# Performance work log

Measured on AMD Instinct MI355X. Metric: run time of the kernel, lower is better.

The kernel has to match this reference:

```python
import jax, jax.numpy as jnp
import numpy as np

HIDDEN = 2048
N_HEADS = 16
HEAD_DIM = HIDDEN // N_HEADS
ROPE_BASE = 10000.0


def rotate_half(x):
    half = x.shape[-1] // 2
    return jnp.concatenate((-x[..., half:], x[..., :half]), axis=-1)


def rope_cos_sin(seq_len, dtype):
    inv_freq = 1.0 / (ROPE_BASE ** (jnp.arange(0, HEAD_DIM, 2, dtype=jnp.float32) / HEAD_DIM))
    pos = jnp.arange(seq_len, dtype=jnp.float32)
    freqs = jnp.einsum('i,j->ij', pos, inv_freq)  # [S, hd/2]
    emb = jnp.concatenate((freqs, freqs), axis=-1)  # [S, hd]
    return jnp.cos(emb).astype(dtype), jnp.sin(emb).astype(dtype)


def setup_inputs() -> dict:
    key = jax.random.key(0)
    ks = jax.random.split(key, 9)
    B, S, H = 2, 2048, HIDDEN
    std = 1.0 / np.sqrt(H)
    return {
        'hidden_states': jax.random.normal(ks[0], (B, S, H), dtype=jnp.float32),
        'Wq': jax.random.uniform(ks[1], (H, H), jnp.float32, -std, std),
        'bq': jax.random.uniform(ks[2], (H,), jnp.float32, -std, std),
        'Wk': jax.random.uniform(ks[3], (H, H), jnp.float32, -std, std),
        'bk': jax.random.uniform(ks[4], (H,), jnp.float32, -std, std),
        'Wv': jax.random.uniform(ks[5], (H, H), jnp.float32, -std, std),
        'bv': jax.random.uniform(ks[6], (H,), jnp.float32, -std, std),
        'Wo': jax.random.uniform(ks[7], (H, H), jnp.float32, -std, std),
        'bo': jax.random.uniform(ks[8], (H,), jnp.float32, -std, std),
    }


def reference(hidden_states, Wq, bq, Wk, bk, Wv, bv, Wo, bo):
    B, S, H = hidden_states.shape
    scale = HEAD_DIM ** -0.5

    def proj(W, b):
        # torch Linear: x @ W.T + b
        y = jnp.einsum('bsh,oh->bso', hidden_states, W) + b
        return y.reshape(B, S, N_HEADS, HEAD_DIM).transpose(0, 2, 1, 3)  # [B,nh,S,hd]

    q = proj(Wq, bq)
    k = proj(Wk, bk)
    v = proj(Wv, bv)

    cos, sin = rope_cos_sin(S, hidden_states.dtype)  # [S, hd]
    cos = cos[None, None, :, :]
    sin = sin[None, None, :, :]
    q = q * cos + rotate_half(q) * sin
    k = k * cos + rotate_half(k) * sin

    scores = jnp.einsum('bhqd,bhkd->bhqk', q, k) * scale  # [B,nh,S,S]
    probs = jax.nn.softmax(scores, axis=-1)
    ctx = jnp.einsum('bhqk,bhkd->bhqd', probs, v)
    ctx = ctx.transpose(0, 2, 1, 3).reshape(B, S, H)
    return jnp.einsum('bsh,oh->bso', ctx, Wo) + bo
```

## Files before the change

kernel.cpp:

```cpp
#include <hip/hip_runtime.h>
#include <hip/hip_bf16.h>
#include <math.h>

#define HIDDEN 2048
#define NH 16
#define HD 128
#define NB 2
#define SEQ 2048
#define K_DIM 2048

typedef unsigned int u32;
typedef unsigned short ushort_t;
typedef __bf16 bf16x8 __attribute__((ext_vector_type(8)));
typedef float f32x4 __attribute__((ext_vector_type(4)));
typedef ushort_t u16x8 __attribute__((ext_vector_type(8)));

__device__ __forceinline__ void split1(float x, unsigned short& h, unsigned short& l) {
    u32 u = __float_as_uint(x);
    u32 hr = (u + 0x7FFFu + ((u >> 16) & 1u)) >> 16;
    h = (unsigned short)hr;
    float r = x - __uint_as_float(hr << 16);
    u32 u2 = __float_as_uint(r);
    l = (unsigned short)((u2 + 0x7FFFu + ((u2 >> 16) & 1u)) >> 16);
}

__device__ __forceinline__ ushort_t bf16r(float x) {
    u32 u = __float_as_uint(x);
    return (ushort_t)((u + 0x7FFFu + ((u >> 16) & 1u)) >> 16);
}

__device__ __forceinline__ float bf2f(ushort_t u) {
    return __uint_as_float(((u32)u) << 16);
}

__device__ __forceinline__ void gl_lds16(const void* g, void* l) {
    __builtin_amdgcn_global_load_lds(
        (const __attribute__((address_space(1))) u32*)g,
        (__attribute__((address_space(3))) u32*)l, 16, 0, 0);
}

#define XG 2097152
#define WG 1048576
#define TBLK 512
__global__ void k_cvt_all(const float4* __restrict__ X, const float4* __restrict__ W0,
                          const float4* __restrict__ W1, const float4* __restrict__ W2,
                          const float4* __restrict__ Wo,
                          ushort4* __restrict__ Xh, ushort4* __restrict__ H0,
                          ushort4* __restrict__ H1, ushort4* __restrict__ H2,
                          ushort4* __restrict__ WoH, ushort4* __restrict__ WoL,
                          float* __restrict__ ct, float* __restrict__ st) {
    const int blk = blockIdx.x;
    if (blk < TBLK) {
        int idx = blk * 256 + threadIdx.x;
        int s = idx >> 6, d = idx & 63;
        double inv = pow(10000.0, -(double)d * (1.0 / 64.0));
        double ang = (double)s * inv;
        ct[idx] = (float)cos(ang);
        st[idx] = (float)sin(ang);
        return;
    }
    int idx = (blk - TBLK) * 256 + threadIdx.x;
    if (idx < XG + 3 * WG) {
        const float4* src;
        ushort4* dst;
        int off;
        if (idx < XG) { src = X; dst = Xh; off = idx; }
        else {
            int t = idx - XG;
            int m = t >> 20;
            off = t & (WG - 1);
            src = (m == 0) ? W0 : (m == 1) ? W1 : W2;
            dst = (m == 0) ? H0 : (m == 1) ? H1 : H2;
        }
        float4 x = src[off];
        ushort4 h;
        h.x = bf16r(x.x); h.y = bf16r(x.y); h.z = bf16r(x.z); h.w = bf16r(x.w);
        dst[off] = h;
    } else {
        int off = idx - XG - 3 * WG;
        float4 x = Wo[off];
        ushort4 h, l;
        split1(x.x, h.x, l.x);
        split1(x.y, h.y, l.y);
        split1(x.z, h.z, l.z);
        split1(x.w, h.w, l.w);
        WoH[off] = h;
        WoL[off] = l;
    }
}

#define BAR  __builtin_amdgcn_s_barrier()
#define VM6  asm volatile("s_waitcnt vmcnt(6)" ::: "memory")
#define VM4  asm volatile("s_waitcnt vmcnt(4)" ::: "memory")
#define VM0  asm volatile("s_waitcnt vmcnt(0)" ::: "memory")
#define PRIO1 __builtin_amdgcn_s_setprio(1)
#define PRIO0 __builtin_amdgcn_s_setprio(0)

#define QSTAGE(slot, kt) do { \
    const ushort_t* gA_ = Xh + sgA + (size_t)(kt) * 32; \
    gl_lds16(gA_, &As[slot][(w * 32) * 32]); \
    gl_lds16(gA_ + 16 * 2048, &As[slot][(w * 32 + 16) * 32]); \
    const ushort_t* gB_ = Wsel + sgB + (size_t)(kt) * 32; \
    gl_lds16(gB_, &Bs[slot][(w * 32) * 32]); \
    gl_lds16(gB_ + 16 * 2048, &Bs[slot][(w * 32 + 16) * 32]); \
} while (0)

#define QRD(AD, BD, slot) do { \
    _Pragma("unroll") for (int mf = 0; mf < 8; mf++) \
        AD[mf] = *(const bf16x8*)&As[slot][arow + mf * 512 + ccq]; \
    _Pragma("unroll") for (int nf = 0; nf < 4; nf++) \
        BD[nf] = *(const bf16x8*)&Bs[slot][brow + nf * 512 + ccq]; \
} while (0)

#define QMFMA(AD, BD) do { PRIO1; \
    _Pragma("unroll") for (int mf = 0; mf < 8; mf++) \
    _Pragma("unroll") for (int nf = 0; nf < 4; nf++) \
        acc[mf][nf] = __builtin_amdgcn_mfma_f32_16x16x32_bf16( \
            AD[mf], BD[nf], acc[mf][nf], 0, 0, 0); \
    PRIO0; } while (0)

__global__ __launch_bounds__(512, 2)
void k_gemm_qkv8(const ushort_t* __restrict__ Xh,
                 const ushort_t* __restrict__ W0, const ushort_t* __restrict__ W1,
                 const ushort_t* __restrict__ W2,
                 const float* __restrict__ b0, const float* __restrict__ b1,
                 const float* __restrict__ b2,
                 ushort_t* __restrict__ o0, ushort_t* __restrict__ o1,
                 ushort_t* __restrict__ o2) {
    __shared__ ushort_t As[4][256 * 32];
    __shared__ ushort_t Bs[4][256 * 32];
    const int tid = threadIdx.x;
    const int lane = tid & 63;
    const int w = tid >> 6;
    const int wm = w >> 2;
    const int wn = w & 3;
    const int quad = lane >> 4;
    const int l15 = lane & 15;

    const int by = blockIdx.x & 7;
    const int t = blockIdx.x >> 3;
    const int mat = t % 3;
    const int m0 = (t / 3) << 8;
    const int n0 = by << 8;
    const ushort_t* Wsel = (mat == 0) ? W0 : (mat == 1) ? W1 : W2;
    const float* bias = (mat == 0) ? b0 : (mat == 1) ? b1 : b2;
    ushort_t* out = (mat == 0) ? o0 : (mat == 1) ? o1 : o2;

    const int lrow4 = lane >> 2;
    const int col8 = (((lane & 3) ^ ((lrow4 >> 1) & 3)) << 3);
    const size_t sgA = (size_t)(m0 + w * 32 + lrow4) * 2048 + col8;
    const size_t sgB = (size_t)(n0 + w * 32 + lrow4) * 2048 + col8;

    const int arow = (wm * 128 + l15) * 32;
    const int brow = (wn * 64 + l15) * 32;
    const int ccq = ((quad ^ ((l15 >> 1) & 3)) << 3);

    f32x4 acc[8][4];
#pragma unroll
    for (int i = 0; i < 8; i++)
#pragma unroll
        for (int j = 0; j < 4; j++) acc[i][j] = (f32x4){0.f, 0.f, 0.f, 0.f};

    bf16x8 aA[8], bA[4], aB[8], bB[4];

    QSTAGE(0, 0); QSTAGE(1, 1);
    VM4; BAR;
    QRD(aA, bA, 0);

    for (int p = 0; p < 60; p += 4) {
        QSTAGE(2, p + 2); VM4; BAR; QRD(aB, bB, 1); QMFMA(aA, bA);
        QSTAGE(3, p + 3); VM4; BAR; QRD(aA, bA, 2); QMFMA(aB, bB);
        QSTAGE(0, p + 4); VM4; BAR; QRD(aB, bB, 3); QMFMA(aA, bA);
        QSTAGE(1, p + 5); VM4; BAR; QRD(aA, bA, 0); QMFMA(aB, bB);
    }
    QSTAGE(2, 62); VM4; BAR; QRD(aB, bB, 1); QMFMA(aA, bA);
    QSTAGE(3, 63); VM4; BAR; QRD(aA, bA, 2); QMFMA(aB, bB);
    VM0; BAR;                QRD(aB, bB, 3); QMFMA(aA, bA);
    QMFMA(aB, bB);

    float bcolv[4];
#pragma unroll
    for (int nf = 0; nf < 4; nf++) bcolv[nf] = bias[n0 + wn * 64 + nf * 16 + l15];

    const int mbase = m0 + wm * 128 + quad * 4;
#pragma unroll
    for (int mf = 0; mf < 8; mf++)
#pragma unroll
        for (int nf = 0; nf < 4; nf++) {
            const int n = n0 + wn * 64 + nf * 16 + l15;
            const int hh = n >> 7;
            const int d = n & 127;
#pragma unroll
            for (int r = 0; r < 4; r++) {
                const int m = mbase + mf * 16 + r;
                const int bb = m >> 11;
                const int s = m & (SEQ - 1);
                out[((size_t)(bb * NH + hh) * SEQ + s) * HD + d] =
                    bf16r(acc[mf][nf][r] + bcolv[nf]);
            }
        }
}

#define OSTAGE(slot, kt) do { \
    const size_t koA = (size_t)((kt) >> 2) * ((size_t)SEQ * HD) + (size_t)((kt) & 3) * 32; \
    const size_t koB = (size_t)(kt) * 32; \
    gl_lds16(Ah + sgA0 + koA, &Ah_s[slot][(w * 32) * 32]); \
    gl_lds16(Ah + sgA0 + 16 * HD + koA, &Ah_s[slot][(w * 32 + 16) * 32]); \
    gl_lds16(Al + sgA0 + koA, &Al_s[slot][(w * 32) * 32]); \
    gl_lds16(Al + sgA0 + 16 * HD + koA, &Al_s[slot][(w * 32 + 16) * 32]); \
    gl_lds16(Bh + sgB0 + koB, &Bh_s[slot][(w * 16) * 32]); \
    gl_lds16(Bl + sgB0 + koB, &Bl_s[slot][(w * 16) * 32]); \
} while (0)

#define ORD(AH, AL, BH, BL, slot) do { \
    _Pragma("unroll") for (int f = 0; f < 4; f++) { \
        AH[f] = *(const bf16x8*)&Ah_s[slot][aro + f * 512 + cco]; \
        AL[f] = *(const bf16x8*)&Al_s[slot][aro + f * 512 + cco]; \
        BH[f] = *(const bf16x8*)&Bh_s[slot][bro + f * 512 + cco]; \
        BL[f] = *(const bf16x8*)&Bl_s[slot][bro + f * 512 + cco]; \
    } \
} while (0)

#define OMFMA(AH, AL, BH, BL) do { PRIO1; \
    _Pragma("unroll") for (int mf = 0; mf < 4; mf++) \
    _Pragma("unroll") for (int nf = 0; nf < 4; nf++) { \
        acc[mf][nf] = __builtin_amdgcn_mfma_f32_16x16x32_bf16( \
            AH[mf], BH[nf], acc[mf][nf], 0, 0, 0); \
        acc[mf][nf] = __builtin_amdgcn_mfma_f32_16x16x32_bf16( \
            AH[mf], BL[nf], acc[mf][nf], 0, 0, 0); \
        acc[mf][nf] = __builtin_amdgcn_mfma_f32_16x16x32_bf16( \
            AL[mf], BH[nf], acc[mf][nf], 0, 0, 0); \
    } PRIO0; } while (0)

__global__ __launch_bounds__(512, 2)
void k_gemm_o2(const ushort_t* __restrict__ Ah, const ushort_t* __restrict__ Al,
               const ushort_t* __restrict__ Bh, const ushort_t* __restrict__ Bl,
               const float* __restrict__ bias, float* __restrict__ out) {
    __shared__ ushort_t Ah_s[3][256 * 32];
    __shared__ ushort_t Al_s[3][256 * 32];
    __shared__ ushort_t Bh_s[3][128 * 32];
    __shared__ ushort_t Bl_s[3][128 * 32];
    const int tid = threadIdx.x;
    const int lane = tid & 63;
    const int w = tid >> 6;
    const int wm = w >> 1;
    const int wn = w & 1;
    const int quad = lane >> 4;
    const int l15 = lane & 15;

    int bid = blockIdx.x;
    bid = (bid & 7) * 32 + (bid >> 3);
    const int bx = bid & 15;
    const int by = bid >> 4;
    const int m0 = bx << 8;
    const int n0 = by << 7;

    const int lrow4 = lane >> 2;
    const int col8 = (((lane & 3) ^ ((lrow4 >> 1) & 3)) << 3);
    const size_t sgA0 = ((size_t)(m0 >> 11) * NH * SEQ + (size_t)((m0 & (SEQ - 1)) + w * 32 + lrow4)) * HD + col8;
    const size_t sgB0 = (size_t)(n0 + w * 16 + lrow4) * K_DIM + col8;

    const int aro = (wm * 64 + l15) * 32;
    const int bro = (wn * 64 + l15) * 32;
    const int cco = ((quad ^ ((l15 >> 1) & 3)) << 3);

    f32x4 acc[4][4];
#pragma unroll
    for (int i = 0; i < 4; i++)
#pragma unroll
        for (int j = 0; j < 4; j++) acc[i][j] = (f32x4){0.f, 0.f, 0.f, 0.f};

    bf16x8 ahA[4], alA[4], bhA[4], blA[4];
    bf16x8 ahB[4], alB[4], bhB[4], blB[4];

    OSTAGE(0, 0);
    OSTAGE(1, 1);
    VM6; BAR;
    ORD(ahA, alA, bhA, blA, 0);

    for (int it = 0; it < 10; ++it) {
        const int q = 6 * it;
        VM0; BAR; OSTAGE(2, q + 2); ORD(ahB, alB, bhB, blB, 1); OMFMA(ahA, alA, bhA, blA);
        VM0; BAR; OSTAGE(0, q + 3); ORD(ahA, alA, bhA, blA, 2); OMFMA(ahB, alB, bhB, blB);
        VM0; BAR; OSTAGE(1, q + 4); ORD(ahB, alB, bhB, blB, 0); OMFMA(ahA, alA, bhA, blA);
        VM0; BAR; OSTAGE(2, q + 5); ORD(ahA, alA, bhA, blA, 1); OMFMA(ahB, alB, bhB, blB);
        VM0; BAR; OSTAGE(0, q + 6); ORD(ahB, alB, bhB, blB, 2); OMFMA(ahA, alA, bhA, blA);
        VM0; BAR; OSTAGE(1, q + 7); ORD(ahA, alA, bhA, blA, 0); OMFMA(ahB, alB, bhB, blB);
    }
    VM0; BAR; OSTAGE(2, 62); ORD(ahB, alB, bhB, blB, 1); OMFMA(ahA, alA, bhA, blA);
    VM0; BAR; OSTAGE(0, 63); ORD(ahA, alA, bhA, blA, 2); OMFMA(ahB, alB, bhB, blB);
    VM0; BAR;                ORD(ahB, alB, bhB, blB, 0); OMFMA(ahA, alA, bhA, blA);
    OMFMA(ahB, alB, bhB, blB);

    float bcolv[4];
#pragma unroll
    for (int nf = 0; nf < 4; nf++) bcolv[nf] = bias[n0 + wn * 64 + nf * 16 + l15];

    const int mb = m0 + wm * 64 + quad * 4;
    const int nb = n0 + wn * 64 + l15;
#pragma unroll
    for (int fm = 0; fm < 4; fm++)
#pragma unroll
        for (int fn = 0; fn < 4; fn++)
#pragma unroll
            for (int r = 0; r < 4; r++)
                out[(size_t)(mb + fm * 16 + r) * HIDDEN + nb + fn * 16] =
                    acc[fm][fn][r] + bcolv[fn];
}

__global__ __launch_bounds__(256)
void k_ropek_vpack(const ushort_t* __restrict__ kb, const ushort_t* __restrict__ vb,
                   const float* __restrict__ ct, const float* __restrict__ st,
                   ushort_t* __restrict__ Kb, ushort_t* __restrict__ vt) {
    __shared__ float t[64][65];
    const int tid = threadIdx.x;
    const int blk = blockIdx.x;
    if (blk < 2048) {
        int idx = blk * 256 + tid;
        int o = idx & 7;
        int s = (idx >> 3) & (SEQ - 1);
        int bh = idx >> 14;
        const int d0 = o << 3;
        size_t base = ((size_t)bh * SEQ + s) * HD;
        float c[8], sn[8];
        *(float4*)&c[0]  = *(const float4*)&ct[(s << 6) + d0];
        *(float4*)&c[4]  = *(const float4*)&ct[(s << 6) + d0 + 4];
        *(float4*)&sn[0] = *(const float4*)&st[(s << 6) + d0];
        *(float4*)&sn[4] = *(const float4*)&st[(s << 6) + d0 + 4];
        u16x8 k0 = *(const u16x8*)(kb + base + d0);
        u16x8 k1 = *(const u16x8*)(kb + base + 64 + d0);
        u16x8 lo, hi;
#pragma unroll
        for (int j = 0; j < 8; j++) {
            float a = bf2f(k0[j]), b = bf2f(k1[j]);
            lo[j] = bf16r(a * c[j] - b * sn[j]);
            hi[j] = bf16r(b * c[j] + a * sn[j]);
        }
        *(u16x8*)(Kb + base + d0) = lo;
        *(u16x8*)(Kb + base + 64 + d0) = hi;
    } else {
        int b = blk - 2048;
        const int s0 = (b & 31) << 6;
        const int d0 = ((b >> 5) & 1) << 6;
        const int bh = b >> 6;
        const ushort_t* src = vb + ((size_t)bh * SEQ + s0) * HD + d0;
        const int rr = tid >> 4;
        const int cc = (tid & 15) << 2;
#pragma unroll
        for (int i = 0; i < 4; i++) {
            ushort4 x = *(const ushort4*)(src + (size_t)(i * 16 + rr) * HD + cc);
            t[i * 16 + rr][cc]     = bf2f(x.x);
            t[i * 16 + rr][cc + 1] = bf2f(x.y);
            t[i * 16 + rr][cc + 2] = bf2f(x.z);
            t[i * 16 + rr][cc + 3] = bf2f(x.w);
        }
        __syncthreads();
        const int dr = tid >> 2;
        const int sc_ = (tid & 3) << 4;
        ushort_t* dst = vt + ((size_t)bh * HD + d0 + dr) * SEQ + s0 + sc_;
        u16x8 o0, o1;
#pragma unroll
        for (int u = 0; u < 8; u++) o0[u] = bf16r(t[sc_ + u][dr]);
#pragma unroll
        for (int u = 0; u < 8; u++) o1[u] = bf16r(t[sc_ + 8 + u][dr]);
        *(u16x8*)dst = o0;
        *(u16x8*)(dst + 8) = o1;
    }
}

__global__ __launch_bounds__(512, 1)
void k_flash_mfma(const ushort_t* __restrict__ Qb, const ushort_t* __restrict__ Kb,
                  const ushort_t* __restrict__ Vt,
                  const float* __restrict__ ct, const float* __restrict__ st,
                  ushort_t* __restrict__ ch, ushort_t* __restrict__ cl) {
    __shared__ ushort_t SH[36352];
    ushort_t* Ks = SH;
    ushort_t* Vs = SH + 8704;
    ushort_t* Ps = SH + 17920;
    const int tid = threadIdx.x;
    const int lane = tid & 63;
    const int w = tid >> 6;
    const int quad = lane >> 4;
    const int l15 = lane & 15;
    const int bi = blockIdx.x;
    const int bh = bi & 31;
    const int qt = bi >> 5;
    const ushort_t* Qg = Qb + ((size_t)bh * SEQ + ((size_t)qt << 8)) * HD;
    const ushort_t* Kg = Kb + (size_t)bh * SEQ * HD;
    const ushort_t* Vg = Vt + (size_t)bh * HD * SEQ;

    const float scq = 0.08838834764831845f;
    bf16x8 qf[2][4];
#pragma unroll
    for (int qi = 0; qi < 2; qi++) {
        const int row = w * 32 + qi * 16 + l15;
        const int sg = (qt << 8) + row;
        const int tb = (sg << 6) + quad * 8;
        float c0[8], s0[8], c1[8], s1[8];
        *(float4*)&c0[0] = *(const float4*)&ct[tb];
        *(float4*)&c0[4] = *(const float4*)&ct[tb + 4];
        *(float4*)&s0[0] = *(const float4*)&st[tb];
        *(float4*)&s0[4] = *(const float4*)&st[tb + 4];
        *(float4*)&c1[0] = *(const float4*)&ct[tb + 32];
        *(float4*)&c1[4] = *(const float4*)&ct[tb + 36];
        *(float4*)&s1[0] = *(const float4*)&st[tb + 32];
        *(float4*)&s1[4] = *(const float4*)&st[tb + 36];
        const ushort_t* qrow = Qg + (size_t)row * HD + quad * 8;
        u16x8 r0 = *(const u16x8*)(qrow);
        u16x8 r1 = *(const u16x8*)(qrow + 32);
        u16x8 r2 = *(const u16x8*)(qrow + 64);
        u16x8 r3 = *(const u16x8*)(qrow + 96);
        u16x8 f0, f1, f2, f3;
#pragma unroll
        for (int j = 0; j < 8; j++) {
            float a0 = bf2f(r0[j]), a1 = bf2f(r1[j]);
            float a2 = bf2f(r2[j]), a3 = bf2f(r3[j]);
            f0[j] = bf16r((a0 * c0[j] - a2 * s0[j]) * scq);
            f2[j] = bf16r((a2 * c0[j] + a0 * s0[j]) * scq);
            f1[j] = bf16r((a1 * c1[j] - a3 * s1[j]) * scq);
            f3[j] = bf16r((a3 * c1[j] + a1 * s1[j]) * scq);
        }
        qf[qi][0] = __builtin_bit_cast(bf16x8, f0);
        qf[qi][1] = __builtin_bit_cast(bf16x8, f1);
        qf[qi][2] = __builtin_bit_cast(bf16x8, f2);
        qf[qi][3] = __builtin_bit_cast(bf16x8, f3);
    }

    const int sr = tid >> 4;
    const int sc8 = (tid & 15) << 3;
    const int vr = tid >> 3;
    const int vc8 = (tid & 7) << 3;

    u16x8 Kreg[2], Vreg[2];
#pragma unroll
    for (int i = 0; i < 2; i++)
        Kreg[i] = *(const u16x8*)(Kg + (size_t)(i * 32 + sr) * HD + sc8);
#pragma unroll
    for (int i = 0; i < 2; i++)
        Vreg[i] = *(const u16x8*)(Vg + (size_t)(i * 64 + vr) * SEQ + vc8);

    f32x4 acc[2][8];
#pragma unroll
    for (int qi = 0; qi < 2; qi++)
#pragma unroll
        for (int d = 0; d < 8; d++) acc[qi][d] = (f32x4){0.f, 0.f, 0.f, 0.f};
    float lp[2] = {0.f, 0.f};

    for (int kt = 0; kt < SEQ; kt += 64) {
        const int np = kt + 64;
        __syncthreads();
#pragma unroll
        for (int i = 0; i < 2; i++)
            *(u16x8*)&Ks[(i * 32 + sr) * 136 + sc8] = Kreg[i];
#pragma unroll
        for (int i = 0; i < 2; i++)
            *(u16x8*)&Vs[(i * 64 + vr) * 72 + vc8] = Vreg[i];
        if (np < SEQ) {
#pragma unroll
            for (int i = 0; i < 2; i++)
                Kreg[i] = *(const u16x8*)(Kg + (size_t)(np + i * 32 + sr) * HD + sc8);
#pragma unroll
            for (int i = 0; i < 2; i++)
                Vreg[i] = *(const u16x8*)(Vg + (size_t)(i * 64 + vr) * SEQ + np + vc8);
        }
        __syncthreads();

        f32x4 sc[2][4];
#pragma unroll
        for (int qi = 0; qi < 2; qi++)
#pragma unroll
            for (int j = 0; j < 4; j++) sc[qi][j] = (f32x4){0.f, 0.f, 0.f, 0.f};
#pragma unroll
        for (int ks = 0; ks < 4; ks++) {
            bf16x8 kf[4];
#pragma unroll
            for (int j = 0; j < 4; j++)
                kf[j] = *(const bf16x8*)&Ks[(j * 16 + l15) * 136 + ks * 32 + quad * 8];
#pragma unroll
            for (int qi = 0; qi < 2; qi++)
#pragma unroll
                for (int j = 0; j < 4; j++)
                    sc[qi][j] = __builtin_amdgcn_mfma_f32_16x16x32_bf16(
                        kf[j], qf[qi][ks], sc[qi][j], 0, 0, 0);
        }

#pragma unroll
        for (int qi = 0; qi < 2; qi++) {
            const int prow = (w * 32 + qi * 16 + l15) * 72 + quad * 4;
#pragma unroll
            for (int j = 0; j < 4; j++) {
                float p0 = __expf(sc[qi][j][0]);
                float p1 = __expf(sc[qi][j][1]);
                float p2 = __expf(sc[qi][j][2]);
                float p3 = __expf(sc[qi][j][3]);
                lp[qi] += (p0 + p1) + (p2 + p3);
                __hip_bfloat162 lo2 = __float22bfloat162_rn({p0, p1});
                __hip_bfloat162 hi2 = __float22bfloat162_rn({p2, p3});
                uint2 pk = make_uint2(*(u32*)&lo2, *(u32*)&hi2);
                *(uint2*)&Ps[prow + j * 16] = pk;
            }
        }

#pragma unroll
        for (int ks = 0; ks < 2; ks++) {
            bf16x8 pf[2];
#pragma unroll
            for (int qi = 0; qi < 2; qi++)
                pf[qi] = *(const bf16x8*)&Ps[(w * 32 + qi * 16 + l15) * 72 + ks * 32 + quad * 8];
#pragma unroll
            for (int db = 0; db < 8; db++) {
                bf16x8 vf = *(const bf16x8*)&Vs[(db * 16 + l15) * 72 + ks * 32 + quad * 8];
#pragma unroll
                for (int qi = 0; qi < 2; qi++)
                    acc[qi][db] = __builtin_amdgcn_mfma_f32_16x16x32_bf16(vf, pf[qi], acc[qi][db], 0, 0, 0);
            }
        }
    }

    float inv[2];
#pragma unroll
    for (int qi = 0; qi < 2; qi++) {
        float l = lp[qi];
        l += __shfl_xor(l, 16);
        l += __shfl_xor(l, 32);
        inv[qi] = 1.0f / l;
    }
    const size_t obase = ((size_t)bh * SEQ + ((size_t)qt << 8)) * HD;

    __syncthreads();
#pragma unroll
    for (int qi = 0; qi < 2; qi++)
#pragma unroll
        for (int db = 0; db < 8; db++) {
            ushort4 hh;
            ushort_t dum;
            split1(acc[qi][db][0] * inv[qi], hh.x, dum);
            split1(acc[qi][db][1] * inv[qi], hh.y, dum);
            split1(acc[qi][db][2] * inv[qi], hh.z, dum);
            split1(acc[qi][db][3] * inv[qi], hh.w, dum);
            *(ushort4*)&SH[(w * 32 + qi * 16 + l15) * 136 + db * 16 + quad * 4] = hh;
        }
    __syncthreads();
#pragma unroll
    for (int t2 = 0; t2 < 8; t2++) {
        int c = t2 * 512 + tid;
        int row = c >> 4, col8 = (c & 15) << 3;
        *(u16x8*)&ch[obase + (size_t)row * HD + col8] = *(const u16x8*)&SH[row * 136 + col8];
    }
    __syncthreads();
#pragma unroll
    for (int qi = 0; qi < 2; qi++)
#pragma unroll
        for (int db = 0; db < 8; db++) {
            ushort4 ll;
            ushort_t dum;
            split1(acc[qi][db][0] * inv[qi], dum, ll.x);
            split1(acc[qi][db][1] * inv[qi], dum, ll.y);
            split1(acc[qi][db][2] * inv[qi], dum, ll.z);
            split1(acc[qi][db][3] * inv[qi], dum, ll.w);
            *(ushort4*)&SH[(w * 32 + qi * 16 + l15) * 136 + db * 16 + quad * 4] = ll;
        }
    __syncthreads();
#pragma unroll
    for (int t2 = 0; t2 < 8; t2++) {
        int c = t2 * 512 + tid;
        int row = c >> 4, col8 = (c & 15) << 3;
        *(u16x8*)&cl[obase + (size_t)row * HD + col8] = *(const u16x8*)&SH[row * 136 + col8];
    }
}

extern "C" void kernel_launch(void* const* d_in, const int* in_sizes, int n_in,
                              void* d_out, int out_size, void* d_ws, size_t ws_size,
                              hipStream_t stream) {
    const float* X  = (const float*)d_in[0];
    const float* Wq = (const float*)d_in[1];
    const float* bq = (const float*)d_in[2];
    const float* Wk = (const float*)d_in[3];
    const float* bk = (const float*)d_in[4];
    const float* Wv = (const float*)d_in[5];
    const float* bv = (const float*)d_in[6];
    const float* Wo = (const float*)d_in[7];
    const float* bo = (const float*)d_in[8];
    float* out = (float*)d_out;

    const size_t QS = (size_t)NB * NH * SEQ * HD;
    const size_t WS = (size_t)HIDDEN * HIDDEN;
    ushort_t* qb_ws = (ushort_t*)d_ws;
    ushort_t* kb_ws = qb_ws + QS;
    ushort_t* vb_ws = kb_ws + QS;
    float* cost = (float*)(vb_ws + QS);
    float* sint = cost + (size_t)SEQ * 64;
    ushort_t* Xh = (ushort_t*)(sint + (size_t)SEQ * 64);
    ushort_t* Wh0 = Xh + QS;
    ushort_t* Wh1 = Wh0 + WS;
    ushort_t* Wh2 = Wh1 + WS;
    ushort_t* Woh = Wh2 + WS;
    ushort_t* Wol = Woh + WS;
    ushort_t* Kb  = Wol + WS;
    ushort_t* Vtb = Kb + QS;
    ushort_t* ctxh = Xh;
    ushort_t* ctxl = kb_ws;

    k_cvt_all<<<TBLK + (XG + 4 * WG) / 256, 256, 0, stream>>>(
        (const float4*)X, (const float4*)Wq, (const float4*)Wk, (const float4*)Wv,
        (const float4*)Wo,
        (ushort4*)Xh, (ushort4*)Wh0, (ushort4*)Wh1, (ushort4*)Wh2,
        (ushort4*)Woh, (ushort4*)Wol, cost, sint);

    k_gemm_qkv8<<<384, 512, 0, stream>>>(Xh, Wh0, Wh1, Wh2, bq, bk, bv,
                                         qb_ws, kb_ws, vb_ws);

    k_ropek_vpack<<<4096, 256, 0, stream>>>(kb_ws, vb_ws, cost, sint, Kb, Vtb);

    k_flash_mfma<<<256, 512, 0, stream>>>(qb_ws, Kb, Vtb, cost, sint, ctxh, ctxl);

    k_gemm_o2<<<dim3(256), 512, 0, stream>>>(ctxh, ctxl, Woh, Wol, bo, out);
}
```

Baseline: 454.2 us.

## Fuse K RoPE into QKV GEMM epilogue via LDS partner exchange

Moves the rotary embedding for K out of the separate ropek/vpack kernel and into the QKV GEMM epilogue. The K tile's rotate-half partner values are swapped through a padded shared-memory buffer, then rotated and written straight into the final K buffer. This removes one global read and write pass over K and the rope half of the follow-up kernel, which now only transposes V. In exchange the LDS layout is merged and enlarged and the launch bound drops to one block per SM, which may reduce occupancy in the GEMM main loop.

```diff
diff --git a/kernel.cpp b/kernel.cpp
--- a/kernel.cpp
+++ b/kernel.cpp
@@ -96,20 +96,24 @@
 #define PRIO1 __builtin_amdgcn_s_setprio(1)
 #define PRIO0 __builtin_amdgcn_s_setprio(0)
 
+#define AS_(slot) (shAll + (slot) * 8192)
+#define BS_(slot) (shAll + 32768 + (slot) * 8192)
+#define XPAD 260
+
 #define QSTAGE(slot, kt) do { \
     const ushort_t* gA_ = Xh + sgA + (size_t)(kt) * 32; \
-    gl_lds16(gA_, &As[slot][(w * 32) * 32]); \
-    gl_lds16(gA_ + 16 * 2048, &As[slot][(w * 32 + 16) * 32]); \
+    gl_lds16(gA_, AS_(slot) + (w * 32) * 32); \
+    gl_lds16(gA_ + 16 * 2048, AS_(slot) + (w * 32 + 16) * 32); \
     const ushort_t* gB_ = Wsel + sgB + (size_t)(kt) * 32; \
-    gl_lds16(gB_, &Bs[slot][(w * 32) * 32]); \
-    gl_lds16(gB_ + 16 * 2048, &Bs[slot][(w * 32 + 16) * 32]); \
+    gl_lds16(gB_, BS_(slot) + (w * 32) * 32); \
+    gl_lds16(gB_ + 16 * 2048, BS_(slot) + (w * 32 + 16) * 32); \
 } while (0)
 
 #define QRD(AD, BD, slot) do { \
     _Pragma("unroll") for (int mf = 0; mf < 8; mf++) \
-        AD[mf] = *(const bf16x8*)&As[slot][arow + mf * 512 + ccq]; \
+        AD[mf] = *(const bf16x8*)&AS_(slot)[arow + mf * 512 + ccq]; \
     _Pragma("unroll") for (int nf = 0; nf < 4; nf++) \
-        BD[nf] = *(const bf16x8*)&Bs[slot][brow + nf * 512 + ccq]; \
+        BD[nf] = *(const bf16x8*)&BS_(slot)[brow + nf * 512 + ccq]; \
 } while (0)
 
 #define QMFMA(AD, BD) do { PRIO1; \
@@ -119,16 +123,16 @@
             AD[mf], BD[nf], acc[mf][nf], 0, 0, 0); \
     PRIO0; } while (0)
 
-__global__ __launch_bounds__(512, 2)
+__global__ __launch_bounds__(512, 1)
 void k_gemm_qkv8(const ushort_t* __restrict__ Xh,
                  const ushort_t* __restrict__ W0, const ushort_t* __restrict__ W1,
                  const ushort_t* __restrict__ W2,
                  const float* __restrict__ b0, const float* __restrict__ b1,
                  const float* __restrict__ b2,
+                 const float* __restrict__ ct, const float* __restrict__ st,
                  ushort_t* __restrict__ o0, ushort_t* __restrict__ o1,
                  ushort_t* __restrict__ o2) {
-    __shared__ ushort_t As[4][256 * 32];
-    __shared__ ushort_t Bs[4][256 * 32];
+    __shared__ ushort_t shAll[256 * XPAD];
     const int tid = threadIdx.x;
     const int lane = tid & 63;
     const int w = tid >> 6;
@@ -183,22 +187,78 @@
     for (int nf = 0; nf < 4; nf++) bcolv[nf] = bias[n0 + wn * 64 + nf * 16 + l15];
 
     const int mbase = m0 + wm * 128 + quad * 4;
+
+    ushort4 me[8][4];
 #pragma unroll
     for (int mf = 0; mf < 8; mf++)
 #pragma unroll
         for (int nf = 0; nf < 4; nf++) {
-            const int n = n0 + wn * 64 + nf * 16 + l15;
-            const int hh = n >> 7;
-            const int d = n & 127;
-#pragma unroll
-            for (int r = 0; r < 4; r++) {
-                const int m = mbase + mf * 16 + r;
-                const int bb = m >> 11;
-                const int s = m & (SEQ - 1);
-                out[((size_t)(bb * NH + hh) * SEQ + s) * HD + d] =
-                    bf16r(acc[mf][nf][r] + bcolv[nf]);
+            me[mf][nf].x = bf16r(acc[mf][nf][0] + bcolv[nf]);
+            me[mf][nf].y = bf16r(acc[mf][nf][1] + bcolv[nf]);
+            me[mf][nf].z = bf16r(acc[mf][nf][2] + bcolv[nf]);
+            me[mf][nf].w = bf16r(acc[mf][nf][3] + bcolv[nf]);
+        }
+
+    if (mat != 1) {
+#pragma unroll
+        for (int mf = 0; mf < 8; mf++)
+#pragma unroll
+            for (int nf = 0; nf < 4; nf++) {
+                const int n = n0 + wn * 64 + nf * 16 + l15;
+                const int hh = n >> 7;
+                const int d = n & 127;
+                const ushort_t vv[4] = {me[mf][nf].x, me[mf][nf].y,
+                                        me[mf][nf].z, me[mf][nf].w};
+#pragma unroll
+                for (int r = 0; r < 4; r++) {
+                    const int m = mbase + mf * 16 + r;
+                    const int bb = m >> 11;
+                    const int s = m & (SEQ - 1);
+                    out[((size_t)(bb * NH + hh) * SEQ + s) * HD + d] = vv[r];
+                }
             }
-        }
+    } else {
+        BAR;
+#pragma unroll
+        for (int mf = 0; mf < 8; mf++) {
+            const int mloc = wm * 128 + mf * 16 + quad * 4;
+#pragma unroll
+            for (int nf = 0; nf < 4; nf++) {
+                const int nloc = wn * 64 + nf * 16 + l15;
+                *(ushort4*)&shAll[nloc * XPAD + mloc] = me[mf][nf];
+            }
+        }
+        BAR;
+#pragma unroll
+        for (int mf = 0; mf < 8; mf++) {
+            const int mloc = wm * 128 + mf * 16 + quad * 4;
+#pragma unroll
+            for (int nf = 0; nf < 4; nf++) {
+                const int nloc = wn * 64 + nf * 16 + l15;
+                ushort4 pr = *(const ushort4*)&shAll[(nloc ^ 64) * XPAD + mloc];
+                const int n = n0 + nloc;
+                const int hh = n >> 7;
+                const int d = n & 127;
+                const int ddx = nf * 16 + l15;
+                const ushort_t mev[4] = {me[mf][nf].x, me[mf][nf].y,
+                                         me[mf][nf].z, me[mf][nf].w};
+                const ushort_t prv[4] = {pr.x, pr.y, pr.z, pr.w};
+#pragma unroll
+                for (int r = 0; r < 4; r++) {
+                    const int m = mbase + mf * 16 + r;
+                    const int bb = m >> 11;
+                    const int s = m & (SEQ - 1);
+                    const float c = ct[(s << 6) + ddx];
+                    const float sn = st[(s << 6) + ddx];
+                    const float a = bf2f(mev[r]);
+                    const float b = bf2f(prv[r]);
+                    const float v = (wn & 1) ? (a * c + b * sn)
+                                             : (a * c - b * sn);
+                    out[((size_t)(bb * NH + hh) * SEQ + s) * HD + d] = bf16r(v);
+                }
+            }
+        }
+    }
 }
 
 #define OSTAGE(slot, kt) do { \
@@ -309,63 +369,35 @@
 }
 
 __global__ __launch_bounds__(256)
-void k_ropek_vpack(const ushort_t* __restrict__ kb, const ushort_t* __restrict__ vb,
-                   const float* __restrict__ ct, const float* __restrict__ st,
-                   ushort_t* __restrict__ Kb, ushort_t* __restrict__ vt) {
+void k_vpack(const ushort_t* __restrict__ vb, ushort_t* __restrict__ vt) {
     __shared__ float t[64][65];
     const int tid = threadIdx.x;
-    const int blk = blockIdx.x;
-    if (blk < 2048) {
-        int idx = blk * 256 + tid;
-        int o = idx & 7;
-        int s = (idx >> 3) & (SEQ - 1);
-        int bh = idx >> 14;
-        const int d0 = o << 3;
-        size_t base = ((size_t)bh * SEQ + s) * HD;
-        float c[8], sn[8];
-        *(float4*)&c[0]  = *(const float4*)&ct[(s << 6) + d0];
-        *(float4*)&c[4]  = *(const float4*)&ct[(s << 6) + d0 + 4];
-        *(float4*)&sn[0] = *(const float4*)&st[(s << 6) + d0];
-        *(float4*)&sn[4] = *(const float4*)&st[(s << 6) + d0 + 4];
-        u16x8 k0 = *(const u16x8*)(kb + base + d0);
-        u16x8 k1 = *(const u16x8*)(kb + base + 64 + d0);
-        u16x8 lo, hi;
-#pragma unroll
-        for (int j = 0; j < 8; j++) {
-            float a = bf2f(k0[j]), b = bf2f(k1[j]);
-            lo[j] = bf16r(a * c[j] - b * sn[j]);
-            hi[j] = bf16r(b * c[j] + a * sn[j]);
-        }
-        *(u16x8*)(Kb + base + d0) = lo;
-        *(u16x8*)(Kb + base + 64 + d0) = hi;
-    } else {
-        int b = blk - 2048;
-        const int s0 = (b & 31) << 6;
-        const int d0 = ((b >> 5) & 1) << 6;
-        const int bh = b >> 6;
-        const ushort_t* src = vb + ((size_t)bh * SEQ + s0) * HD + d0;
-        const int rr = tid >> 4;
-        const int cc = (tid & 15) << 2;
-#pragma unroll
-        for (int i = 0; i < 4; i++) {
-            ushort4 x = *(const ushort4*)(src + (size_t)(i * 16 + rr) * HD + cc);
-            t[i * 16 + rr][cc]     = bf2f(x.x);
-            t[i * 16 + rr][cc + 1] = bf2f(x.y);
-            t[i * 16 + rr][cc + 2] = bf2f(x.z);
-            t[i * 16 + rr][cc + 3] = bf2f(x.w);
-        }
-        __syncthreads();
-        const int dr = tid >> 2;
-        const int sc_ = (tid & 3) << 4;
-        ushort_t* dst = vt + ((size_t)bh * HD + d0 + dr) * SEQ + s0 + sc_;
-        u16x8 o0, o1;
-#pragma unroll
-        for (int u = 0; u < 8; u++) o0[u] = bf16r(t[sc_ + u][dr]);
-#pragma unroll
-        for (int u = 0; u < 8; u++) o1[u] = bf16r(t[sc_ + 8 + u][dr]);
-        *(u16x8*)dst = o0;
-        *(u16x8*)(dst + 8) = o1;
-    }
+    const int b = blockIdx.x;
+    const int s0 = (b & 31) << 6;
+    const int d0 = ((b >> 5) & 1) << 6;
+    const int bh = b >> 6;
+    const ushort_t* src = vb + ((size_t)bh * SEQ + s0) * HD + d0;
+    const int rr = tid >> 4;
+    const int cc = (tid & 15) << 2;
+#pragma unroll
+    for (int i = 0; i < 4; i++) {
+        ushort4 x = *(const ushort4*)(src + (size_t)(i * 16 + rr) * HD + cc);
+        t[i * 16 + rr][cc]     = bf2f(x.x);
+        t[i * 16 + rr][cc + 1] = bf2f(x.y);
+        t[i * 16 + rr][cc + 2] = bf2f(x.z);
+        t[i * 16 + rr][cc + 3] = bf2f(x.w);
+    }
+    __syncthreads();
+    const int dr = tid >> 2;
+    const int sc_ = (tid & 3) << 4;
+    ushort_t* dst = vt + ((size_t)bh * HD + d0 + dr) * SEQ + s0 + sc_;
+    u16x8 o0, o1;
+#pragma unroll
+    for (int u = 0; u < 8; u++) o0[u] = bf16r(t[sc_ + u][dr]);
+#pragma unroll
+    for (int u = 0; u < 8; u++) o1[u] = bf16r(t[sc_ + 8 + u][dr]);
+    *(u16x8*)dst = o0;
+    *(u16x8*)(dst + 8) = o1;
 }
 
 __global__ __launch_bounds__(512, 1)
@@ -608,9 +640,9 @@
         (ushort4*)Woh, (ushort4*)Wol, cost, sint);
 
     k_gemm_qkv8<<<384, 512, 0, stream>>>(Xh, Wh0, Wh1, Wh2, bq, bk, bv,
-                                         qb_ws, kb_ws, vb_ws);
-
-    k_ropek_vpack<<<4096, 256, 0, stream>>>(kb_ws, vb_ws, cost, sint, Kb, Vtb);
+                                         cost, sint, qb_ws, Kb, vb_ws);
+
+    k_vpack<<<2048, 256, 0, stream>>>(vb_ws, Vtb);
 
     k_flash_mfma<<<256, 512, 0, stream>>>(qb_ws, Kb, Vtb, cost, sint, ctxh, ctxl);
 
```

Result: slower. 479.1 us (+5.5%).
